# Kernel optimization log

Measured on AMD Instinct MI355X. Metric: run time of the kernel, lower is better.

Reference implementation:

```python
import jax, jax.numpy as jnp
import numpy as np

T_DIFF = 1000.0
LN_EPS = 1e-5


def _lin(x, w, b):
    return jnp.matmul(x, w.T) + b


def _ln(x, g, b):
    m = jnp.mean(x, axis=-1, keepdims=True)
    v = jnp.mean((x - m) ** 2, axis=-1, keepdims=True)
    return (x - m) / jnp.sqrt(v + LN_EPS) * g + b


def _pos_lin(x, w, b):
    return jnp.matmul(x, jax.nn.softplus(w).T) + b


def _gamma(t, g_l1_w, g_l1_b, g_l2_w, g_l2_b, g_l3_w, g_l3_b, gamma_0, gamma_1):
    def gtilde(u):
        l1 = _pos_lin(u, g_l1_w, g_l1_b)
        return l1 + _pos_lin(jax.nn.sigmoid(_pos_lin(l1, g_l2_w, g_l2_b)), g_l3_w, g_l3_b)
    g0, g1, gt = gtilde(jnp.zeros_like(t)), gtilde(jnp.ones_like(t)), gtilde(t)
    return gamma_0 + (gamma_1 - gamma_0) * (gt - g0) / (g1 - g0)


def _pair_dist(a):
    # safe pairwise euclidean distances, (B,N,N,1)
    diff = a[:, :, None, :] - a[:, None, :, :]
    d2 = jnp.sum(diff * diff, axis=-1, keepdims=True)
    return diff, jnp.sqrt(jnp.maximum(d2, 1e-12)), d2


def _egc_layer(x, h, x0, p):
    _, d0, _ = _pair_dist(x0)                      # original distances
    diff, dist, d2 = _pair_dist(x)                 # current distances (pre-LN x)
    h = _ln(h, p['lnh_g'], p['lnh_b'])
    x = _ln(x, p['lnx_g'], p['lnx_b'])
    B, N, F = h.shape
    h_i = jnp.broadcast_to(h[:, :, None, :], (B, N, N, F))
    h_j = jnp.broadcast_to(h[:, None, :, :], (B, N, N, F))
    einp = jnp.concatenate([h_i, h_j, d2, d0], axis=-1)  # (B,N,N,2F+2)
    m = jax.nn.silu(_lin(einp, p['edg1_w'], p['edg1_b']))
    m = jax.nn.silu(_lin(m, p['edg2_w'], p['edg2_b']))
    e = jax.nn.sigmoid(_lin(m, p['edgi_w'], p['edgi_b']))
    e = e * (1.0 - jnp.eye(N, dtype=e.dtype)[None, :, :, None])
    m_agg = jnp.sum(e * m, axis=2)                 # sum over j -> (B,N,F)
    hn = jax.nn.silu(_lin(jnp.concatenate([h, m_agg], axis=-1), p['node1_w'], p['node1_b']))
    hn = h + _lin(hn, p['node2_w'], p['node2_b'])
    cw = jax.nn.silu(_lin(einp, p['cor1_w'], p['cor1_b']))
    cw = jax.nn.silu(_lin(cw, p['cor2_w'], p['cor2_b']))
    cw = _lin(cw, p['cor3_w'], p['cor3_b'])        # (B,N,N,1)
    x_next = x + jnp.sum(cw * (diff / (dist + 1.0)), axis=2)
    return x_next, hn


def setup_inputs() -> dict:
    key = jax.random.key(0)
    ks = iter(jax.random.split(key, 64))
    B, N, H, L = 8, 192, 32, 4
    d = {}
    d['xyz_atom_species'] = jax.random.normal(next(ks), (B, N, 4), jnp.float32)
    d['pdf'] = jax.random.normal(next(ks), (B, 3000), jnp.float32)
    d['t'] = jax.random.uniform(next(ks), (B,), jnp.float32) * T_DIFF

    def w(k, shape):
        fan_in = shape[-1]
        return jax.random.normal(k, shape, jnp.float32) / np.sqrt(fan_in)

    d['emb_in_w'] = w(next(ks), (H, 12)); d['emb_in_b'] = jnp.zeros((H,), jnp.float32)
    d['emb_out_w'] = w(next(ks), (1, H)); d['emb_out_b'] = jnp.zeros((1,), jnp.float32)
    d['x_out_w'] = w(next(ks), (3, 3)); d['x_out_b'] = jnp.zeros((3,), jnp.float32)
    d['pdf_w'] = w(next(ks), (10, 3000)); d['pdf_b'] = jnp.zeros((10,), jnp.float32)
    d['g_l1_w'] = w(next(ks), (1, 1)); d['g_l1_b'] = jnp.zeros((1,), jnp.float32)
    d['g_l2_w'] = w(next(ks), (1024, 1)); d['g_l2_b'] = jnp.zeros((1024,), jnp.float32)
    d['g_l3_w'] = w(next(ks), (1, 1024)); d['g_l3_b'] = jnp.zeros((1,), jnp.float32)
    d['gamma_0'] = jnp.array([-5.0], jnp.float32)
    d['gamma_1'] = jnp.array([10.0], jnp.float32)
    d['lnh_g'] = jnp.ones((L, H), jnp.float32); d['lnh_b'] = jnp.zeros((L, H), jnp.float32)
    d['lnx_g'] = jnp.ones((L, 3), jnp.float32); d['lnx_b'] = jnp.zeros((L, 3), jnp.float32)
    d['edg1_w'] = w(next(ks), (L, H, 2 * H + 2)); d['edg1_b'] = jnp.zeros((L, H), jnp.float32)
    d['edg2_w'] = w(next(ks), (L, H, H)); d['edg2_b'] = jnp.zeros((L, H), jnp.float32)
    d['edgi_w'] = w(next(ks), (L, 1, H)); d['edgi_b'] = jnp.zeros((L, 1), jnp.float32)
    d['node1_w'] = w(next(ks), (L, H, 2 * H)); d['node1_b'] = jnp.zeros((L, H), jnp.float32)
    d['node2_w'] = w(next(ks), (L, H, H)); d['node2_b'] = jnp.zeros((L, H), jnp.float32)
    d['cor1_w'] = w(next(ks), (L, H, 2 * H + 2)); d['cor1_b'] = jnp.zeros((L, H), jnp.float32)
    d['cor2_w'] = w(next(ks), (L, H, H)); d['cor2_b'] = jnp.zeros((L, H), jnp.float32)
    d['cor3_w'] = w(next(ks), (L, 1, H)); d['cor3_b'] = jnp.zeros((L, 1), jnp.float32)
    return d


def reference(xyz_atom_species, pdf, t, emb_in_w, emb_in_b, emb_out_w, emb_out_b,
              x_out_w, x_out_b, pdf_w, pdf_b, g_l1_w, g_l1_b, g_l2_w, g_l2_b,
              g_l3_w, g_l3_b, gamma_0, gamma_1, lnh_g, lnh_b, lnx_g, lnx_b,
              edg1_w, edg1_b, edg2_w, edg2_b, edgi_w, edgi_b, node1_w, node1_b,
              node2_w, node2_b, cor1_w, cor1_b, cor2_w, cor2_b, cor3_w, cor3_b):
    B, N, _ = xyz_atom_species.shape
    h = xyz_atom_species[:, :, 3:4]                # (B,N,1)
    x = xyz_atom_species[:, :, :3]
    x0 = x
    tn = (t / T_DIFF)[:, None]                     # (B,1)
    t_emb = _gamma(tn, g_l1_w, g_l1_b, g_l2_w, g_l2_b, g_l3_w, g_l3_b, gamma_0, gamma_1)
    pdf_emb = _lin(pdf, pdf_w, pdf_b)              # (B,10)
    h = jnp.concatenate([
        h,
        jnp.broadcast_to(t_emb[:, None, :], (B, N, 1)),
        jnp.broadcast_to(pdf_emb[:, None, :], (B, N, 10)),
    ], axis=-1)
    h = _lin(h, emb_in_w, emb_in_b)                # (B,N,32)
    for l in range(4):
        p = dict(lnh_g=lnh_g[l], lnh_b=lnh_b[l], lnx_g=lnx_g[l], lnx_b=lnx_b[l],
                 edg1_w=edg1_w[l], edg1_b=edg1_b[l], edg2_w=edg2_w[l], edg2_b=edg2_b[l],
                 edgi_w=edgi_w[l], edgi_b=edgi_b[l], node1_w=node1_w[l], node1_b=node1_b[l],
                 node2_w=node2_w[l], node2_b=node2_b[l], cor1_w=cor1_w[l], cor1_b=cor1_b[l],
                 cor2_w=cor2_w[l], cor2_b=cor2_b[l], cor3_w=cor3_w[l], cor3_b=cor3_b[l])
        x, h = _egc_layer(x, h, x0, p)
    h = _lin(h, emb_out_w, emb_out_b)
    x = _lin(x, x_out_w, x_out_b) - x0
    return jnp.concatenate([x, h], axis=-1)        # (B,N,4)
```

## Files before the change

### kernel.cpp

```cpp
#include <hip/hip_runtime.h>
#include <hip/hip_bf16.h>
#include <math.h>

#define BATCH 8
#define NATOMS 192
#define HF 32

using short8 = __attribute__((ext_vector_type(8))) short;
using f32x4  = __attribute__((ext_vector_type(4))) float;

__device__ __forceinline__ float fast_rcp(float x){ return __builtin_amdgcn_rcpf(x); }
__device__ __forceinline__ float sigmoid_f(float x){ return fast_rcp(1.0f+__expf(-x)); }
__device__ __forceinline__ float silu_f(float x){ return x*fast_rcp(1.0f+__expf(-x)); }
__device__ __forceinline__ float softplus_f(float x){ return fmaxf(x,0.0f)+log1pf(expf(-fabsf(x))); }
__device__ __forceinline__ unsigned short f2bf(float x){
  __hip_bfloat16 h = __float2bfloat16(x);
  return __builtin_bit_cast(unsigned short, h);
}

__device__ __forceinline__ float wave_sum(float v){
  v += __shfl_xor(v, 1);
  v += __shfl_xor(v, 2);
  v += __shfl_xor(v, 4);
  v += __shfl_xor(v, 8);
  v += __shfl_xor(v, 16);
  v += __shfl_xor(v, 32);
  return v;
}

__global__ __launch_bounds__(256) void k_prelude(
    const float* __restrict__ pdf, const float* __restrict__ t,
    const float* __restrict__ pdf_w, const float* __restrict__ pdf_b,
    const float* __restrict__ g1w, const float* __restrict__ g1b,
    const float* __restrict__ g2w, const float* __restrict__ g2b,
    const float* __restrict__ g3w, const float* __restrict__ g3b,
    const float* __restrict__ gamma0, const float* __restrict__ gamma1,
    float* __restrict__ temb, float* __restrict__ pdfe)
{
  __shared__ float lds[4];
  const int bx = blockIdx.x, tid = threadIdx.x;
  const int wv = tid >> 6, ln = tid & 63;

  if (bx < 80){
    const int b = bx / 10, o = bx % 10;
    const float* pb = pdf + b*3000;
    const float* wb = pdf_w + o*3000;
    float p = 0.f;
    for (int k = tid; k < 3000; k += 256) p = fmaf(pb[k], wb[k], p);
    p = wave_sum(p);
    if (ln == 0) lds[wv] = p;
    __syncthreads();
    if (tid == 0) pdfe[b*10 + o] = lds[0] + lds[1] + lds[2] + lds[3] + pdf_b[o];
    return;
  }
  const int b = bx - 80;
  const float w1 = softplus_f(g1w[0]);
  const float b1 = g1b[0];
  const float tn = t[b] * (1.0f/1000.0f);
  const float l1_0 = b1;
  const float l1_1 = w1 + b1;
  const float l1_t = fmaf(w1, tn, b1);
  float a0 = 0.f, a1 = 0.f, at = 0.f;
  for (int k = tid; k < 1024; k += 256){
    float w2 = softplus_f(g2w[k]);
    float bb = g2b[k];
    float w3 = softplus_f(g3w[k]);
    a0 += sigmoid_f(fmaf(w2, l1_0, bb)) * w3;
    a1 += sigmoid_f(fmaf(w2, l1_1, bb)) * w3;
    at += sigmoid_f(fmaf(w2, l1_t, bb)) * w3;
  }
  float sums[3]; float vals[3] = {a0, a1, at};
  for (int r = 0; r < 3; ++r){
    float v = wave_sum(vals[r]);
    __syncthreads();
    if (ln == 0) lds[wv] = v;
    __syncthreads();
    sums[r] = lds[0] + lds[1] + lds[2] + lds[3];
  }
  if (tid == 0){
    const float b3 = g3b[0];
    const float g0 = l1_0 + sums[0] + b3;
    const float g1v = l1_1 + sums[1] + b3;
    const float gt = l1_t + sums[2] + b3;
    temb[b] = gamma0[0] + (gamma1[0] - gamma0[0]) * (gt - g0) / (g1v - g0);
  }
}

__global__ __launch_bounds__(256) void k_embed(
    const float* __restrict__ xyz, const float* __restrict__ temb,
    const float* __restrict__ pdfe, const float* __restrict__ wi,
    const float* __restrict__ bi, float* __restrict__ h, float* __restrict__ x)
{
  int g = blockIdx.x * 256 + threadIdx.x;
  if (g >= BATCH*NATOMS*HF) return;
  int f = g & 31;
  int node = g >> 5;
  int b = node / NATOMS;
  float sp = xyz[node*4 + 3];
  const float* w = wi + f*12;
  float a = bi[f];
  a = fmaf(sp, w[0], a);
  a = fmaf(temb[b], w[1], a);
  const float* pe = pdfe + b*10;
#pragma unroll
  for (int p = 0; p < 10; ++p) a = fmaf(pe[p], w[2+p], a);
  h[node*32 + f] = a;
  if (f < 3) x[node*3 + f] = xyz[node*4 + f];
}

__global__ __launch_bounds__(256) void k_wprep(
    const float* __restrict__ e2w, const float* __restrict__ c2w,
    unsigned short* __restrict__ e2wb, unsigned short* __restrict__ c2wb)
{
  int g = blockIdx.x*256 + threadIdx.x;
  if (g < 4096){
    e2wb[g] = f2bf(e2w[g]);
    c2wb[g] = f2bf(c2w[g]);
  }
}

__global__ __launch_bounds__(256) void k_node(
    const float* __restrict__ hraw,
    const float* __restrict__ lnhg, const float* __restrict__ lnhb,
    const float* __restrict__ e1w, const float* __restrict__ e1b,
    const float* __restrict__ c1w, const float* __restrict__ c1b,
    float* __restrict__ hln, float* __restrict__ ue, float* __restrict__ uc,
    float* __restrict__ vep, float* __restrict__ vcp)
{
  int g = blockIdx.x * 256 + threadIdx.x;
  if (g >= BATCH*NATOMS*32) return;
  const int f = g & 31, node = g >> 5;
  const float* row = hraw + node*32;
  float hl[32];
  float m = 0.f;
#pragma unroll
  for (int k = 0; k < 32; ++k){ hl[k] = row[k]; m += hl[k]; }
  m *= (1.0f/32.0f);
  float v = 0.f;
#pragma unroll
  for (int k = 0; k < 32; ++k){ float d = hl[k]-m; v = fmaf(d, d, v); }
  float r = rsqrtf(v*(1.0f/32.0f) + 1e-5f);
#pragma unroll
  for (int k = 0; k < 32; ++k) hl[k] = fmaf((hl[k]-m)*r, lnhg[k], lnhb[k]);
  hln[node*32 + f] = hl[f];

  const float* we = e1w + f*66;
  float sv = e1b[f], su = 0.f;
#pragma unroll
  for (int k = 0; k < 32; ++k){ sv = fmaf(hl[k], we[k], sv); su = fmaf(hl[k], we[32+k], su); }
  vep[node*32 + f] = sv;
  ue [node*32 + f] = su;

  const float* wc = c1w + f*66;
  float cv = c1b[f], cu = 0.f;
#pragma unroll
  for (int k = 0; k < 32; ++k){ cv = fmaf(hl[k], wc[k], cv); cu = fmaf(hl[k], wc[32+k], cu); }
  vcp[node*32 + f] = cv;
  uc [node*32 + f] = cu;
}

__global__ __launch_bounds__(128, 3) void k_pair(
    const float* __restrict__ xin, const float* __restrict__ xyz,
    const float* __restrict__ ue, const float* __restrict__ uc,
    const float* __restrict__ vep, const float* __restrict__ vcp,
    const float* __restrict__ e1w, const float* __restrict__ c1w,
    const unsigned short* __restrict__ e2wb, const unsigned short* __restrict__ c2wb,
    const float* __restrict__ e2b, const float* __restrict__ eiw,
    const float* __restrict__ eib,
    const float* __restrict__ c2b, const float* __restrict__ c3w,
    const float* __restrict__ c3b,
    float* __restrict__ pm, float* __restrict__ pxc)
{
  __shared__ float s_geo[64][6];
  __shared__ unsigned short s_m1[64][40];
  __shared__ unsigned short s_c1[64][40];
  __shared__ unsigned short s_we[32][40];
  __shared__ unsigned short s_wc[32][40];

  const int i = blockIdx.x, b = blockIdx.y, chunk = blockIdx.z;
  const int tid = threadIdx.x;
  const int base = b * NATOMS;

  if (tid < 64){
    const int jj = tid;
    const int j = chunk*64 + jj;
    const float* xi_p = xin + (base + i)*3;
    const float* xj_p = xin + (base + j)*3;
    const float dfx = xi_p[0] - xj_p[0], dfy = xi_p[1] - xj_p[1], dfz = xi_p[2] - xj_p[2];
    const float d2 = dfx*dfx + dfy*dfy + dfz*dfz;
    const float dist = sqrtf(fmaxf(d2, 1e-12f));
    const float* x0i = xyz + (base + i)*4;
    const float* x0j = xyz + (base + j)*4;
    const float q0 = x0i[0]-x0j[0], q1 = x0i[1]-x0j[1], q2 = x0i[2]-x0j[2];
    const float d0 = sqrtf(fmaxf(q0*q0 + q1*q1 + q2*q2, 1e-12f));
    s_geo[jj][0] = dfx; s_geo[jj][1] = dfy; s_geo[jj][2] = dfz;
    s_geo[jj][3] = d2;  s_geo[jj][4] = d0;  s_geo[jj][5] = dist;
  } else {
    const int u = tid - 64;
    const short8* es = (const short8*)e2wb;
    const short8* cs = (const short8*)c2wb;
#pragma unroll
    for (int h = 0; h < 2; ++h){
      const int c = u + h*64;
      const int f = c >> 2, kq = c & 3;
      *(short8*)&s_we[f][kq*8] = es[c];
      *(short8*)&s_wc[f][kq*8] = cs[c];
    }
  }
  __syncthreads();

  {
    const int k = tid & 31, jg = tid >> 5;
    const float vpe = vep[(base + i)*32 + k];
    const float vpc = vcp[(base + i)*32 + k];
    const float we64 = e1w[k*66 + 64], we65 = e1w[k*66 + 65];
    const float wc64 = c1w[k*66 + 64], wc65 = c1w[k*66 + 65];
#pragma unroll
    for (int jj = jg; jj < 64; jj += 4){
      const float d2 = s_geo[jj][3], d0 = s_geo[jj][4];
      const int j = chunk*64 + jj;
      const float uev = ue[(size_t)(base + j)*32 + k];
      const float m1 = silu_f(fmaf(d2, we64, fmaf(d0, we65, vpe + uev)));
      s_m1[jj][k] = f2bf(m1);
      const float ucv = uc[(size_t)(base + j)*32 + k];
      const float c1 = silu_f(fmaf(d2, wc64, fmaf(d0, wc65, vpc + ucv)));
      s_c1[jj][k] = f2bf(c1);
    }
  }
  __syncthreads();

  const int lane = tid & 63;
  const int n = lane & 15, quad = lane >> 4;

  if (tid < 64){
    short8 b0 = *(const short8*)&s_we[n][quad*8];
    short8 b1 = *(const short8*)&s_we[16 + n][quad*8];
    f32x4 acc0[4], acc1[4];
#pragma unroll
    for (int jt = 0; jt < 4; ++jt){
      short8 a = *(const short8*)&s_m1[jt*16 + n][quad*8];
      f32x4 z = {0.f, 0.f, 0.f, 0.f};
      acc0[jt] = __builtin_amdgcn_mfma_f32_16x16x32_bf16(a, b0, z, 0, 0, 0);
      acc1[jt] = __builtin_amdgcn_mfma_f32_16x16x32_bf16(a, b1, z, 0, 0, 0);
    }
    const float eb0 = e2b[n], eb1 = e2b[16 + n];
    const float ew0 = eiw[n], ew1 = eiw[16 + n];
    const float ebias = eib[0];
    float ma0 = 0.f, ma1 = 0.f;
#pragma unroll
    for (int jt = 0; jt < 4; ++jt){
      float m20[4], m21[4], g[4];
#pragma unroll
      for (int r = 0; r < 4; ++r){
        m20[r] = silu_f(acc0[jt][r] + eb0);
        m21[r] = silu_f(acc1[jt][r] + eb1);
        g[r] = m20[r]*ew0 + m21[r]*ew1;
      }
#pragma unroll
      for (int r = 0; r < 4; ++r){
        g[r] += __shfl_xor(g[r], 1);
        g[r] += __shfl_xor(g[r], 2);
        g[r] += __shfl_xor(g[r], 4);
        g[r] += __shfl_xor(g[r], 8);
      }
#pragma unroll
      for (int r = 0; r < 4; ++r){
        const int jglob = chunk*64 + jt*16 + quad*4 + r;
        const float e = (jglob == i) ? 0.0f : sigmoid_f(g[r] + ebias);
        ma0 = fmaf(e, m20[r], ma0);
        ma1 = fmaf(e, m21[r], ma1);
      }
    }
    ma0 += __shfl_xor(ma0, 16); ma0 += __shfl_xor(ma0, 32);
    ma1 += __shfl_xor(ma1, 16); ma1 += __shfl_xor(ma1, 32);
    if (lane < 16){
      float* o = pm + ((size_t)(base + i)*3 + chunk)*32;
      o[lane] = ma0;
      o[16 + lane] = ma1;
    }
  } else {
    short8 b0 = *(const short8*)&s_wc[n][quad*8];
    short8 b1 = *(const short8*)&s_wc[16 + n][quad*8];
    f32x4 acc0[4], acc1[4];
#pragma unroll
    for (int jt = 0; jt < 4; ++jt){
      short8 a = *(const short8*)&s_c1[jt*16 + n][quad*8];
      f32x4 z = {0.f, 0.f, 0.f, 0.f};
      acc0[jt] = __builtin_amdgcn_mfma_f32_16x16x32_bf16(a, b0, z, 0, 0, 0);
      acc1[jt] = __builtin_amdgcn_mfma_f32_16x16x32_bf16(a, b1, z, 0, 0, 0);
    }
    const float cb0 = c2b[n], cb1 = c2b[16 + n];
    const float cw0 = c3w[n], cw1 = c3w[16 + n];
    const float cbias = c3b[0];
    float px = 0.f, py = 0.f, pz = 0.f;
#pragma unroll
    for (int jt = 0; jt < 4; ++jt){
      float g[4];
#pragma unroll
      for (int r = 0; r < 4; ++r){
        g[r] = silu_f(acc0[jt][r] + cb0)*cw0 + silu_f(acc1[jt][r] + cb1)*cw1;
      }
#pragma unroll
      for (int r = 0; r < 4; ++r){
        g[r] += __shfl_xor(g[r], 1);
        g[r] += __shfl_xor(g[r], 2);
        g[r] += __shfl_xor(g[r], 4);
        g[r] += __shfl_xor(g[r], 8);
      }
#pragma unroll
      for (int r = 0; r < 4; ++r){
        const int jj = jt*16 + quad*4 + r;
        const float s = (g[r] + cbias) * fast_rcp(s_geo[jj][5] + 1.0f);
        px = fmaf(s, s_geo[jj][0], px);
        py = fmaf(s, s_geo[jj][1], py);
        pz = fmaf(s, s_geo[jj][2], pz);
      }
    }
    px += __shfl_xor(px, 16); px += __shfl_xor(px, 32);
    py += __shfl_xor(py, 16); py += __shfl_xor(py, 32);
    pz += __shfl_xor(pz, 16); pz += __shfl_xor(pz, 32);
    if (lane == 0){
      float* o = pxc + ((size_t)(base + i)*3 + chunk)*3;
      o[0] = px; o[1] = py; o[2] = pz;
    }
  }
}

__global__ __launch_bounds__(256) void k_post(
    float* hln, const float* __restrict__ xin,
    const float* __restrict__ pm, const float* __restrict__ pxc,
    float* __restrict__ hout, float* __restrict__ xout,
    const float* __restrict__ n1w, const float* __restrict__ n1b,
    const float* __restrict__ n2w, const float* __restrict__ n2b,
    const float* __restrict__ lnxg, const float* __restrict__ lnxb,
    const float* __restrict__ lnhg_n, const float* __restrict__ lnhb_n,
    const float* __restrict__ e1w_n, const float* __restrict__ e1b_n,
    const float* __restrict__ c1w_n, const float* __restrict__ c1b_n,
    float* __restrict__ ue, float* __restrict__ uc,
    float* __restrict__ vep, float* __restrict__ vcp)
{
  __shared__ float s_hl[8][33];
  __shared__ float s_mg[8][33];
  __shared__ float s_n1[8][33];
  __shared__ float s_ho[8][33];

  const int tid = threadIdx.x;
  const int il = tid >> 5, f = tid & 31;
  const int node = blockIdx.x*8 + il;

  const float hlf = hln[node*32 + f];
  s_hl[il][f] = hlf;
  const float* pmn = pm + (size_t)node*96;
  s_mg[il][f] = pmn[f] + pmn[32 + f] + pmn[64 + f];
  __syncthreads();

  float a = n1b[f];
  const float* w1 = n1w + f*64;
#pragma unroll
  for (int k = 0; k < 32; ++k) a = fmaf(s_hl[il][k], w1[k], a);
#pragma unroll
  for (int k = 0; k < 32; ++k) a = fmaf(s_mg[il][k], w1[32+k], a);
  s_n1[il][f] = silu_f(a);

  if (f < 3){
    const float* xr = xin + node*3;
    const float x0 = xr[0], x1 = xr[1], x2 = xr[2];
    const float mx = (x0 + x1 + x2) * (1.0f/3.0f);
    const float v0 = x0-mx, v1 = x1-mx, v2 = x2-mx;
    const float r = rsqrtf((v0*v0 + v1*v1 + v2*v2)*(1.0f/3.0f) + 1e-5f);
    const float xv = (f == 0) ? x0 : ((f == 1) ? x1 : x2);
    const float xl = fmaf((xv - mx)*r, lnxg[f], lnxb[f]);
    const float* pc = pxc + (size_t)node*9;
    xout[node*3 + f] = xl + pc[f] + pc[3 + f] + pc[6 + f];
  }
  __syncthreads();

  float o = n2b[f];
  const float* w2 = n2w + f*32;
#pragma unroll
  for (int k = 0; k < 32; ++k) o = fmaf(s_n1[il][k], w2[k], o);
  const float ho = hlf + o;
  hout[node*32 + f] = ho;
  s_ho[il][f] = ho;
  __syncthreads();

  float m = 0.f;
#pragma unroll
  for (int k = 0; k < 32; ++k) m += s_ho[il][k];
  m *= (1.0f/32.0f);
  float v = 0.f;
#pragma unroll
  for (int k = 0; k < 32; ++k){ float d = s_ho[il][k]-m; v = fmaf(d, d, v); }
  const float r = rsqrtf(v*(1.0f/32.0f) + 1e-5f);
  float hl[32];
#pragma unroll
  for (int k = 0; k < 32; ++k) hl[k] = fmaf((s_ho[il][k]-m)*r, lnhg_n[k], lnhb_n[k]);
  hln[node*32 + f] = hl[f];

  const float* we = e1w_n + f*66;
  float sv = e1b_n[f], su = 0.f;
#pragma unroll
  for (int k = 0; k < 32; ++k){ sv = fmaf(hl[k], we[k], sv); su = fmaf(hl[k], we[32+k], su); }
  vep[node*32 + f] = sv;
  ue [node*32 + f] = su;

  const float* wc = c1w_n + f*66;
  float cv = c1b_n[f], cu = 0.f;
#pragma unroll
  for (int k = 0; k < 32; ++k){ cv = fmaf(hl[k], wc[k], cv); cu = fmaf(hl[k], wc[32+k], cu); }
  vcp[node*32 + f] = cv;
  uc [node*32 + f] = cu;
}

__global__ __launch_bounds__(256) void k_final(
    const float* __restrict__ hin, const float* __restrict__ xin,
    const float* __restrict__ xyz,
    const float* __restrict__ how, const float* __restrict__ hob,
    const float* __restrict__ xow, const float* __restrict__ xob,
    float* __restrict__ out)
{
  int g = blockIdx.x * 256 + threadIdx.x;
  if (g >= BATCH*NATOMS) return;
  const float* h = hin + g*32;
  float a = hob[0];
#pragma unroll
  for (int k = 0; k < 32; ++k) a = fmaf(h[k], how[k], a);
  const float* x = xin + g*3;
#pragma unroll
  for (int c = 0; c < 3; ++c){
    float o = xob[c];
    o = fmaf(x[0], xow[c*3+0], o);
    o = fmaf(x[1], xow[c*3+1], o);
    o = fmaf(x[2], xow[c*3+2], o);
    out[g*4 + c] = o - xyz[g*4 + c];
  }
  out[g*4 + 3] = a;
}

extern "C" void kernel_launch(void* const* d_in, const int* in_sizes, int n_in,
                              void* d_out, int out_size, void* d_ws, size_t ws_size,
                              hipStream_t stream)
{
  const float* xyz      = (const float*)d_in[0];
  const float* pdf      = (const float*)d_in[1];
  const float* t        = (const float*)d_in[2];
  const float* emb_in_w = (const float*)d_in[3];
  const float* emb_in_b = (const float*)d_in[4];
  const float* emb_out_w= (const float*)d_in[5];
  const float* emb_out_b= (const float*)d_in[6];
  const float* x_out_w  = (const float*)d_in[7];
  const float* x_out_b  = (const float*)d_in[8];
  const float* pdf_w    = (const float*)d_in[9];
  const float* pdf_b    = (const float*)d_in[10];
  const float* g1w      = (const float*)d_in[11];
  const float* g1b      = (const float*)d_in[12];
  const float* g2w      = (const float*)d_in[13];
  const float* g2b      = (const float*)d_in[14];
  const float* g3w      = (const float*)d_in[15];
  const float* g3b      = (const float*)d_in[16];
  const float* gamma0   = (const float*)d_in[17];
  const float* gamma1   = (const float*)d_in[18];
  const float* lnhg     = (const float*)d_in[19];
  const float* lnhb     = (const float*)d_in[20];
  const float* lnxg     = (const float*)d_in[21];
  const float* lnxb     = (const float*)d_in[22];
  const float* e1w      = (const float*)d_in[23];
  const float* e1b      = (const float*)d_in[24];
  const float* e2w      = (const float*)d_in[25];
  const float* e2b      = (const float*)d_in[26];
  const float* eiw      = (const float*)d_in[27];
  const float* eib      = (const float*)d_in[28];
  const float* n1w      = (const float*)d_in[29];
  const float* n1b      = (const float*)d_in[30];
  const float* n2w      = (const float*)d_in[31];
  const float* n2b      = (const float*)d_in[32];
  const float* c1w      = (const float*)d_in[33];
  const float* c1b      = (const float*)d_in[34];
  const float* c2w      = (const float*)d_in[35];
  const float* c2b      = (const float*)d_in[36];
  const float* c3w      = (const float*)d_in[37];
  const float* c3b      = (const float*)d_in[38];

  const int NTOT = BATCH*NATOMS;
  float* ws   = (float*)d_ws;
  float* temb = ws;
  float* pdfe = ws + 8;
  unsigned short* e2wb = (unsigned short*)(ws + 96);
  unsigned short* c2wb = e2wb + 4096;
  float* h0   = ws + 96 + 4096;
  float* hout = h0   + NTOT*32;
  float* xb0  = hout + NTOT*32;
  float* xb1  = xb0  + NTOT*3;
  float* hln  = xb1  + NTOT*3;
  float* ue   = hln  + NTOT*32;
  float* uc   = ue   + NTOT*32;
  float* vep  = uc   + NTOT*32;
  float* vcp  = vep  + NTOT*32;
  float* pm   = vcp  + NTOT*32;
  float* pxc  = pm   + NTOT*96;

  k_prelude<<<88, 256, 0, stream>>>(pdf, t, pdf_w, pdf_b,
      g1w, g1b, g2w, g2b, g3w, g3b, gamma0, gamma1, temb, pdfe);
  k_embed<<<(NTOT*HF + 255)/256, 256, 0, stream>>>(
      xyz, temb, pdfe, emb_in_w, emb_in_b, h0, xb0);
  k_wprep<<<16, 256, 0, stream>>>(e2w, c2w, e2wb, c2wb);
  k_node<<<(NTOT*32 + 255)/256, 256, 0, stream>>>(
      h0, lnhg, lnhb, e1w, e1b, c1w, c1b, hln, ue, uc, vep, vcp);

  const float* xcur = xb0; float* xnext = xb1;
  for (int l = 0; l < 4; ++l){
    const int n = (l < 3) ? (l + 1) : 3;
    k_pair<<<dim3(NATOMS, BATCH, 3), 128, 0, stream>>>(
        xcur, xyz, ue, uc, vep, vcp,
        e1w + l*2112, c1w + l*2112,
        e2wb + l*1024, c2wb + l*1024,
        e2b + l*32, eiw + l*32, eib + l,
        c2b + l*32, c3w + l*32, c3b + l,
        pm, pxc);
    k_post<<<NTOT/8, 256, 0, stream>>>(
        hln, xcur, pm, pxc, hout, xnext,
        n1w + l*2048, n1b + l*32, n2w + l*1024, n2b + l*32,
        lnxg + l*3, lnxb + l*3,
        lnhg + n*32, lnhb + n*32, e1w + n*2112, e1b + n*32,
        c1w + n*2112, c1b + n*32,
        ue, uc, vep, vcp);
    const float* tx = xcur; xcur = xnext; xnext = (float*)tx;
  }

  k_final<<<(NTOT + 255)/256, 256, 0, stream>>>(
      hout, xcur, xyz, emb_out_w, emb_out_b, x_out_w, x_out_b, (float*)d_out);
}
```

Measured before the change: 274.0 us.

## Fuse pair and post kernels per layer, merge prelude/embed/node launches

```diff
diff --git a/kernel.cpp b/kernel.cpp
--- a/kernel.cpp
+++ b/kernel.cpp
@@ -35,12 +35,20 @@
     const float* __restrict__ g2w, const float* __restrict__ g2b,
     const float* __restrict__ g3w, const float* __restrict__ g3b,
     const float* __restrict__ gamma0, const float* __restrict__ gamma1,
-    float* __restrict__ temb, float* __restrict__ pdfe)
+    const float* __restrict__ e2w, const float* __restrict__ c2w,
+    float* __restrict__ temb, float* __restrict__ pdfe,
+    unsigned short* __restrict__ e2wb, unsigned short* __restrict__ c2wb)
 {
   __shared__ float lds[4];
   const int bx = blockIdx.x, tid = threadIdx.x;
   const int wv = tid >> 6, ln = tid & 63;
 
+  if (bx >= 88){
+    const int g = (bx - 88)*256 + tid;
+    e2wb[g] = f2bf(e2w[g]);
+    c2wb[g] = f2bf(c2w[g]);
+    return;
+  }
   if (bx < 80){
     const int b = bx / 10, o = bx % 10;
     const float* pb = pdf + b*3000;
@@ -86,55 +94,37 @@
   }
 }
 
-__global__ __launch_bounds__(256) void k_embed(
+__global__ __launch_bounds__(256) void k_embed_node(
     const float* __restrict__ xyz, const float* __restrict__ temb,
-    const float* __restrict__ pdfe, const float* __restrict__ wi,
-    const float* __restrict__ bi, float* __restrict__ h, float* __restrict__ x)
-{
-  int g = blockIdx.x * 256 + threadIdx.x;
-  if (g >= BATCH*NATOMS*HF) return;
-  int f = g & 31;
-  int node = g >> 5;
-  int b = node / NATOMS;
-  float sp = xyz[node*4 + 3];
-  const float* w = wi + f*12;
-  float a = bi[f];
-  a = fmaf(sp, w[0], a);
-  a = fmaf(temb[b], w[1], a);
-  const float* pe = pdfe + b*10;
-#pragma unroll
-  for (int p = 0; p < 10; ++p) a = fmaf(pe[p], w[2+p], a);
-  h[node*32 + f] = a;
-  if (f < 3) x[node*3 + f] = xyz[node*4 + f];
-}
-
-__global__ __launch_bounds__(256) void k_wprep(
-    const float* __restrict__ e2w, const float* __restrict__ c2w,
-    unsigned short* __restrict__ e2wb, unsigned short* __restrict__ c2wb)
-{
-  int g = blockIdx.x*256 + threadIdx.x;
-  if (g < 4096){
-    e2wb[g] = f2bf(e2w[g]);
-    c2wb[g] = f2bf(c2w[g]);
-  }
-}
-
-__global__ __launch_bounds__(256) void k_node(
-    const float* __restrict__ hraw,
+    const float* __restrict__ pdfe,
+    const float* __restrict__ wi, const float* __restrict__ bi,
     const float* __restrict__ lnhg, const float* __restrict__ lnhb,
     const float* __restrict__ e1w, const float* __restrict__ e1b,
     const float* __restrict__ c1w, const float* __restrict__ c1b,
-    float* __restrict__ hln, float* __restrict__ ue, float* __restrict__ uc,
+    float* __restrict__ x, float* __restrict__ hln,
+    float* __restrict__ ue, float* __restrict__ uc,
     float* __restrict__ vep, float* __restrict__ vcp)
 {
-  int g = blockIdx.x * 256 + threadIdx.x;
-  if (g >= BATCH*NATOMS*32) return;
-  const int f = g & 31, node = g >> 5;
-  const float* row = hraw + node*32;
+  __shared__ float s_h[8][33];
+  const int tid = threadIdx.x;
+  const int il = tid >> 5, f = tid & 31;
+  const int node = blockIdx.x*8 + il;
+  const int b = node / NATOMS;
+  const float* w = wi + f*12;
+  float a = bi[f];
+  a = fmaf(xyz[node*4 + 3], w[0], a);
+  a = fmaf(temb[b], w[1], a);
+  const float* pe = pdfe + b*10;
+#pragma unroll
+  for (int p = 0; p < 10; ++p) a = fmaf(pe[p], w[2+p], a);
+  s_h[il][f] = a;
+  if (f < 3) x[node*3 + f] = xyz[node*4 + f];
+  __syncthreads();
+
   float hl[32];
   float m = 0.f;
 #pragma unroll
-  for (int k = 0; k < 32; ++k){ hl[k] = row[k]; m += hl[k]; }
+  for (int k = 0; k < 32; ++k){ hl[k] = s_h[il][k]; m += hl[k]; }
   m *= (1.0f/32.0f);
   float v = 0.f;
 #pragma unroll
@@ -159,282 +149,260 @@
   uc [node*32 + f] = cu;
 }
 
-__global__ __launch_bounds__(128, 3) void k_pair(
+__global__ __launch_bounds__(128, 3) void k_layer(
     const float* __restrict__ xin, const float* __restrict__ xyz,
     const float* __restrict__ ue, const float* __restrict__ uc,
     const float* __restrict__ vep, const float* __restrict__ vcp,
+    const float* __restrict__ hln,
     const float* __restrict__ e1w, const float* __restrict__ c1w,
     const unsigned short* __restrict__ e2wb, const unsigned short* __restrict__ c2wb,
     const float* __restrict__ e2b, const float* __restrict__ eiw,
     const float* __restrict__ eib,
     const float* __restrict__ c2b, const float* __restrict__ c3w,
     const float* __restrict__ c3b,
-    float* __restrict__ pm, float* __restrict__ pxc)
-{
-  __shared__ float s_geo[64][6];
-  __shared__ unsigned short s_m1[64][40];
-  __shared__ unsigned short s_c1[64][40];
-  __shared__ unsigned short s_we[32][40];
-  __shared__ unsigned short s_wc[32][40];
-
-  const int i = blockIdx.x, b = blockIdx.y, chunk = blockIdx.z;
-  const int tid = threadIdx.x;
-  const int base = b * NATOMS;
-
-  if (tid < 64){
-    const int jj = tid;
-    const int j = chunk*64 + jj;
-    const float* xi_p = xin + (base + i)*3;
-    const float* xj_p = xin + (base + j)*3;
-    const float dfx = xi_p[0] - xj_p[0], dfy = xi_p[1] - xj_p[1], dfz = xi_p[2] - xj_p[2];
-    const float d2 = dfx*dfx + dfy*dfy + dfz*dfz;
-    const float dist = sqrtf(fmaxf(d2, 1e-12f));
-    const float* x0i = xyz + (base + i)*4;
-    const float* x0j = xyz + (base + j)*4;
-    const float q0 = x0i[0]-x0j[0], q1 = x0i[1]-x0j[1], q2 = x0i[2]-x0j[2];
-    const float d0 = sqrtf(fmaxf(q0*q0 + q1*q1 + q2*q2, 1e-12f));
-    s_geo[jj][0] = dfx; s_geo[jj][1] = dfy; s_geo[jj][2] = dfz;
-    s_geo[jj][3] = d2;  s_geo[jj][4] = d0;  s_geo[jj][5] = dist;
-  } else {
-    const int u = tid - 64;
-    const short8* es = (const short8*)e2wb;
-    const short8* cs = (const short8*)c2wb;
-#pragma unroll
-    for (int h = 0; h < 2; ++h){
-      const int c = u + h*64;
-      const int f = c >> 2, kq = c & 3;
-      *(short8*)&s_we[f][kq*8] = es[c];
-      *(short8*)&s_wc[f][kq*8] = cs[c];
-    }
-  }
-  __syncthreads();
-
-  {
-    const int k = tid & 31, jg = tid >> 5;
-    const float vpe = vep[(base + i)*32 + k];
-    const float vpc = vcp[(base + i)*32 + k];
-    const float we64 = e1w[k*66 + 64], we65 = e1w[k*66 + 65];
-    const float wc64 = c1w[k*66 + 64], wc65 = c1w[k*66 + 65];
-#pragma unroll
-    for (int jj = jg; jj < 64; jj += 4){
-      const float d2 = s_geo[jj][3], d0 = s_geo[jj][4];
-      const int j = chunk*64 + jj;
-      const float uev = ue[(size_t)(base + j)*32 + k];
-      const float m1 = silu_f(fmaf(d2, we64, fmaf(d0, we65, vpe + uev)));
-      s_m1[jj][k] = f2bf(m1);
-      const float ucv = uc[(size_t)(base + j)*32 + k];
-      const float c1 = silu_f(fmaf(d2, wc64, fmaf(d0, wc65, vpc + ucv)));
-      s_c1[jj][k] = f2bf(c1);
-    }
-  }
-  __syncthreads();
-
-  const int lane = tid & 63;
-  const int n = lane & 15, quad = lane >> 4;
-
-  if (tid < 64){
-    short8 b0 = *(const short8*)&s_we[n][quad*8];
-    short8 b1 = *(const short8*)&s_we[16 + n][quad*8];
-    f32x4 acc0[4], acc1[4];
-#pragma unroll
-    for (int jt = 0; jt < 4; ++jt){
-      short8 a = *(const short8*)&s_m1[jt*16 + n][quad*8];
-      f32x4 z = {0.f, 0.f, 0.f, 0.f};
-      acc0[jt] = __builtin_amdgcn_mfma_f32_16x16x32_bf16(a, b0, z, 0, 0, 0);
-      acc1[jt] = __builtin_amdgcn_mfma_f32_16x16x32_bf16(a, b1, z, 0, 0, 0);
-    }
-    const float eb0 = e2b[n], eb1 = e2b[16 + n];
-    const float ew0 = eiw[n], ew1 = eiw[16 + n];
-    const float ebias = eib[0];
-    float ma0 = 0.f, ma1 = 0.f;
-#pragma unroll
-    for (int jt = 0; jt < 4; ++jt){
-      float m20[4], m21[4], g[4];
-#pragma unroll
-      for (int r = 0; r < 4; ++r){
-        m20[r] = silu_f(acc0[jt][r] + eb0);
-        m21[r] = silu_f(acc1[jt][r] + eb1);
-        g[r] = m20[r]*ew0 + m21[r]*ew1;
-      }
-#pragma unroll
-      for (int r = 0; r < 4; ++r){
-        g[r] += __shfl_xor(g[r], 1);
-        g[r] += __shfl_xor(g[r], 2);
-        g[r] += __shfl_xor(g[r], 4);
-        g[r] += __shfl_xor(g[r], 8);
-      }
-#pragma unroll
-      for (int r = 0; r < 4; ++r){
-        const int jglob = chunk*64 + jt*16 + quad*4 + r;
-        const float e = (jglob == i) ? 0.0f : sigmoid_f(g[r] + ebias);
-        ma0 = fmaf(e, m20[r], ma0);
-        ma1 = fmaf(e, m21[r], ma1);
-      }
-    }
-    ma0 += __shfl_xor(ma0, 16); ma0 += __shfl_xor(ma0, 32);
-    ma1 += __shfl_xor(ma1, 16); ma1 += __shfl_xor(ma1, 32);
-    if (lane < 16){
-      float* o = pm + ((size_t)(base + i)*3 + chunk)*32;
-      o[lane] = ma0;
-      o[16 + lane] = ma1;
-    }
-  } else {
-    short8 b0 = *(const short8*)&s_wc[n][quad*8];
-    short8 b1 = *(const short8*)&s_wc[16 + n][quad*8];
-    f32x4 acc0[4], acc1[4];
-#pragma unroll
-    for (int jt = 0; jt < 4; ++jt){
-      short8 a = *(const short8*)&s_c1[jt*16 + n][quad*8];
-      f32x4 z = {0.f, 0.f, 0.f, 0.f};
-      acc0[jt] = __builtin_amdgcn_mfma_f32_16x16x32_bf16(a, b0, z, 0, 0, 0);
-      acc1[jt] = __builtin_amdgcn_mfma_f32_16x16x32_bf16(a, b1, z, 0, 0, 0);
-    }
-    const float cb0 = c2b[n], cb1 = c2b[16 + n];
-    const float cw0 = c3w[n], cw1 = c3w[16 + n];
-    const float cbias = c3b[0];
-    float px = 0.f, py = 0.f, pz = 0.f;
-#pragma unroll
-    for (int jt = 0; jt < 4; ++jt){
-      float g[4];
-#pragma unroll
-      for (int r = 0; r < 4; ++r){
-        g[r] = silu_f(acc0[jt][r] + cb0)*cw0 + silu_f(acc1[jt][r] + cb1)*cw1;
-      }
-#pragma unroll
-      for (int r = 0; r < 4; ++r){
-        g[r] += __shfl_xor(g[r], 1);
-        g[r] += __shfl_xor(g[r], 2);
-        g[r] += __shfl_xor(g[r], 4);
-        g[r] += __shfl_xor(g[r], 8);
-      }
-#pragma unroll
-      for (int r = 0; r < 4; ++r){
-        const int jj = jt*16 + quad*4 + r;
-        const float s = (g[r] + cbias) * fast_rcp(s_geo[jj][5] + 1.0f);
-        px = fmaf(s, s_geo[jj][0], px);
-        py = fmaf(s, s_geo[jj][1], py);
-        pz = fmaf(s, s_geo[jj][2], pz);
-      }
-    }
-    px += __shfl_xor(px, 16); px += __shfl_xor(px, 32);
-    py += __shfl_xor(py, 16); py += __shfl_xor(py, 32);
-    pz += __shfl_xor(pz, 16); pz += __shfl_xor(pz, 32);
-    if (lane == 0){
-      float* o = pxc + ((size_t)(base + i)*3 + chunk)*3;
-      o[0] = px; o[1] = py; o[2] = pz;
-    }
-  }
-}
-
-__global__ __launch_bounds__(256) void k_post(
-    float* hln, const float* __restrict__ xin,
-    const float* __restrict__ pm, const float* __restrict__ pxc,
-    float* __restrict__ hout, float* __restrict__ xout,
     const float* __restrict__ n1w, const float* __restrict__ n1b,
     const float* __restrict__ n2w, const float* __restrict__ n2b,
     const float* __restrict__ lnxg, const float* __restrict__ lnxb,
     const float* __restrict__ lnhg_n, const float* __restrict__ lnhb_n,
     const float* __restrict__ e1w_n, const float* __restrict__ e1b_n,
     const float* __restrict__ c1w_n, const float* __restrict__ c1b_n,
-    float* __restrict__ ue, float* __restrict__ uc,
-    float* __restrict__ vep, float* __restrict__ vcp)
+    float* __restrict__ xout, float* __restrict__ hln_n,
+    float* __restrict__ ue_n, float* __restrict__ uc_n,
+    float* __restrict__ vep_n, float* __restrict__ vcp_n,
+    const float* __restrict__ how, const float* __restrict__ hob,
+    const float* __restrict__ xow, const float* __restrict__ xob,
+    float* __restrict__ out, int last)
 {
-  __shared__ float s_hl[8][33];
-  __shared__ float s_mg[8][33];
-  __shared__ float s_n1[8][33];
-  __shared__ float s_ho[8][33];
-
+  __shared__ float s_geo[192][6];
+  __shared__ unsigned short s_m1[64][40];
+  __shared__ unsigned short s_c1[64][40];
+  __shared__ unsigned short s_we[32][40];
+  __shared__ unsigned short s_wc[32][40];
+  __shared__ float s_mg[32];
+  __shared__ float s_hv[32];
+  __shared__ float s_n1[32];
+  __shared__ float s_hl[32];
+
+  const int i = blockIdx.x, b = blockIdx.y;
   const int tid = threadIdx.x;
-  const int il = tid >> 5, f = tid & 31;
-  const int node = blockIdx.x*8 + il;
-
-  const float hlf = hln[node*32 + f];
-  s_hl[il][f] = hlf;
-  const float* pmn = pm + (size_t)node*96;
-  s_mg[il][f] = pmn[f] + pmn[32 + f] + pmn[64 + f];
+  const int base = b * NATOMS;
+
+  {
+    const float* xi_p = xin + (size_t)(base + i)*3;
+    const float xi0 = xi_p[0], xi1 = xi_p[1], xi2 = xi_p[2];
+    const float* x0i = xyz + (size_t)(base + i)*4;
+    const float q0i = x0i[0], q1i = x0i[1], q2i = x0i[2];
+    for (int j = tid; j < NATOMS; j += 128){
+      const float* xj_p = xin + (size_t)(base + j)*3;
+      const float dfx = xi0 - xj_p[0], dfy = xi1 - xj_p[1], dfz = xi2 - xj_p[2];
+      const float d2 = dfx*dfx + dfy*dfy + dfz*dfz;
+      const float dist = sqrtf(fmaxf(d2, 1e-12f));
+      const float* x0j = xyz + (size_t)(base + j)*4;
+      const float q0 = q0i - x0j[0], q1 = q1i - x0j[1], q2 = q2i - x0j[2];
+      const float d0 = sqrtf(fmaxf(q0*q0 + q1*q1 + q2*q2, 1e-12f));
+      s_geo[j][0] = dfx; s_geo[j][1] = dfy; s_geo[j][2] = dfz;
+      s_geo[j][3] = d2;  s_geo[j][4] = d0;  s_geo[j][5] = dist;
+    }
+    const short8* es = (const short8*)e2wb;
+    const short8* cs = (const short8*)c2wb;
+    const int f = tid >> 2, kq = tid & 3;
+    *(short8*)&s_we[f][kq*8] = es[tid];
+    *(short8*)&s_wc[f][kq*8] = cs[tid];
+  }
   __syncthreads();
 
-  float a = n1b[f];
-  const float* w1 = n1w + f*64;
-#pragma unroll
-  for (int k = 0; k < 32; ++k) a = fmaf(s_hl[il][k], w1[k], a);
-#pragma unroll
-  for (int k = 0; k < 32; ++k) a = fmaf(s_mg[il][k], w1[32+k], a);
-  s_n1[il][f] = silu_f(a);
-
-  if (f < 3){
-    const float* xr = xin + node*3;
+  const int kk = tid & 31, jg = tid >> 5;
+  const float vpe = vep[(size_t)(base + i)*32 + kk];
+  const float vpc = vcp[(size_t)(base + i)*32 + kk];
+  const float we64 = e1w[kk*66 + 64], we65 = e1w[kk*66 + 65];
+  const float wc64 = c1w[kk*66 + 64], wc65 = c1w[kk*66 + 65];
+
+  const int lane = tid & 63, wv = tid >> 6;
+  const int n = lane & 15, quad = lane >> 4;
+  short8 wb0, wb1;
+  float p0s, p1s, p2s, p3s, p4s;
+  if (wv == 0){
+    wb0 = *(const short8*)&s_we[n][quad*8];
+    wb1 = *(const short8*)&s_we[16 + n][quad*8];
+    p0s = e2b[n]; p1s = e2b[16 + n]; p2s = eiw[n]; p3s = eiw[16 + n]; p4s = eib[0];
+  } else {
+    wb0 = *(const short8*)&s_wc[n][quad*8];
+    wb1 = *(const short8*)&s_wc[16 + n][quad*8];
+    p0s = c2b[n]; p1s = c2b[16 + n]; p2s = c3w[n]; p3s = c3w[16 + n]; p4s = c3b[0];
+  }
+  float ma0 = 0.f, ma1 = 0.f;
+  float px = 0.f, py = 0.f, pz = 0.f;
+
+  for (int c = 0; c < 3; ++c){
+#pragma unroll
+    for (int jj = jg; jj < 64; jj += 4){
+      const int j = c*64 + jj;
+      const float d2 = s_geo[j][3], d0 = s_geo[j][4];
+      const float uev = ue[(size_t)(base + j)*32 + kk];
+      s_m1[jj][kk] = f2bf(silu_f(fmaf(d2, we64, fmaf(d0, we65, vpe + uev))));
+      const float ucv = uc[(size_t)(base + j)*32 + kk];
+      s_c1[jj][kk] = f2bf(silu_f(fmaf(d2, wc64, fmaf(d0, wc65, vpc + ucv))));
+    }
+    __syncthreads();
+
+    if (wv == 0){
+#pragma unroll
+      for (int jt = 0; jt < 4; ++jt){
+        short8 a = *(const short8*)&s_m1[jt*16 + n][quad*8];
+        f32x4 z = {0.f, 0.f, 0.f, 0.f};
+        f32x4 A0 = __builtin_amdgcn_mfma_f32_16x16x32_bf16(a, wb0, z, 0, 0, 0);
+        f32x4 A1 = __builtin_amdgcn_mfma_f32_16x16x32_bf16(a, wb1, z, 0, 0, 0);
+        float m20[4], m21[4], g[4];
+#pragma unroll
+        for (int r = 0; r < 4; ++r){
+          m20[r] = silu_f(A0[r] + p0s);
+          m21[r] = silu_f(A1[r] + p1s);
+          g[r] = m20[r]*p2s + m21[r]*p3s;
+        }
+#pragma unroll
+        for (int r = 0; r < 4; ++r){
+          g[r] += __shfl_xor(g[r], 1);
+          g[r] += __shfl_xor(g[r], 2);
+          g[r] += __shfl_xor(g[r], 4);
+          g[r] += __shfl_xor(g[r], 8);
+        }
+#pragma unroll
+        for (int r = 0; r < 4; ++r){
+          const int jglob = c*64 + jt*16 + quad*4 + r;
+          const float e = (jglob == i) ? 0.0f : sigmoid_f(g[r] + p4s);
+          ma0 = fmaf(e, m20[r], ma0);
+          ma1 = fmaf(e, m21[r], ma1);
+        }
+      }
+    } else {
+#pragma unroll
+      for (int jt = 0; jt < 4; ++jt){
+        short8 a = *(const short8*)&s_c1[jt*16 + n][quad*8];
+        f32x4 z = {0.f, 0.f, 0.f, 0.f};
+        f32x4 A0 = __builtin_amdgcn_mfma_f32_16x16x32_bf16(a, wb0, z, 0, 0, 0);
+        f32x4 A1 = __builtin_amdgcn_mfma_f32_16x16x32_bf16(a, wb1, z, 0, 0, 0);
+        float g[4];
+#pragma unroll
+        for (int r = 0; r < 4; ++r)
+          g[r] = silu_f(A0[r] + p0s)*p2s + silu_f(A1[r] + p1s)*p3s;
+#pragma unroll
+        for (int r = 0; r < 4; ++r){
+          g[r] += __shfl_xor(g[r], 1);
+          g[r] += __shfl_xor(g[r], 2);
+          g[r] += __shfl_xor(g[r], 4);
+          g[r] += __shfl_xor(g[r], 8);
+        }
+#pragma unroll
+        for (int r = 0; r < 4; ++r){
+          const int jgeo = c*64 + jt*16 + quad*4 + r;
+          const float s = (g[r] + p4s) * fast_rcp(s_geo[jgeo][5] + 1.0f);
+          px = fmaf(s, s_geo[jgeo][0], px);
+          py = fmaf(s, s_geo[jgeo][1], py);
+          pz = fmaf(s, s_geo[jgeo][2], pz);
+        }
+      }
+    }
+    __syncthreads();
+  }
+
+  if (wv == 0){
+    ma0 += __shfl_xor(ma0, 16); ma0 += __shfl_xor(ma0, 32);
+    ma1 += __shfl_xor(ma1, 16); ma1 += __shfl_xor(ma1, 32);
+    if (lane < 16){ s_mg[lane] = ma0; s_mg[16 + lane] = ma1; }
+  } else {
+    px += __shfl_xor(px, 16); px += __shfl_xor(px, 32);
+    py += __shfl_xor(py, 16); py += __shfl_xor(py, 32);
+    pz += __shfl_xor(pz, 16); pz += __shfl_xor(pz, 32);
+    if (lane < 32) s_hv[lane] = hln[(size_t)(base + i)*32 + lane];
+  }
+  __syncthreads();
+
+  if (wv == 0){
+    if (lane < 32){
+      const int f = lane;
+      float a = n1b[f];
+      const float* w1 = n1w + f*64;
+#pragma unroll
+      for (int k = 0; k < 32; ++k) a = fmaf(s_hv[k], w1[k], a);
+#pragma unroll
+      for (int k = 0; k < 32; ++k) a = fmaf(s_mg[k], w1[32+k], a);
+      s_n1[f] = silu_f(a);
+    }
+  } else {
+    const float* xr = xin + (size_t)(base + i)*3;
     const float x0 = xr[0], x1 = xr[1], x2 = xr[2];
     const float mx = (x0 + x1 + x2) * (1.0f/3.0f);
     const float v0 = x0-mx, v1 = x1-mx, v2 = x2-mx;
     const float r = rsqrtf((v0*v0 + v1*v1 + v2*v2)*(1.0f/3.0f) + 1e-5f);
-    const float xv = (f == 0) ? x0 : ((f == 1) ? x1 : x2);
-    const float xl = fmaf((xv - mx)*r, lnxg[f], lnxb[f]);
-    const float* pc = pxc + (size_t)node*9;
-    xout[node*3 + f] = xl + pc[f] + pc[3 + f] + pc[6 + f];
+    const float xn0 = fmaf((x0 - mx)*r, lnxg[0], lnxb[0]) + px;
+    const float xn1 = fmaf((x1 - mx)*r, lnxg[1], lnxb[1]) + py;
+    const float xn2 = fmaf((x2 - mx)*r, lnxg[2], lnxb[2]) + pz;
+    if (!last){
+      if (lane == 0){
+        float* xo = xout + (size_t)(base + i)*3;
+        xo[0] = xn0; xo[1] = xn1; xo[2] = xn2;
+      }
+    } else if (lane < 3){
+      float o = xob[lane];
+      o = fmaf(xn0, xow[lane*3 + 0], o);
+      o = fmaf(xn1, xow[lane*3 + 1], o);
+      o = fmaf(xn2, xow[lane*3 + 2], o);
+      out[(size_t)(base + i)*4 + lane] = o - xyz[(size_t)(base + i)*4 + lane];
+    }
   }
   __syncthreads();
 
-  float o = n2b[f];
-  const float* w2 = n2w + f*32;
-#pragma unroll
-  for (int k = 0; k < 32; ++k) o = fmaf(s_n1[il][k], w2[k], o);
-  const float ho = hlf + o;
-  hout[node*32 + f] = ho;
-  s_ho[il][f] = ho;
-  __syncthreads();
-
-  float m = 0.f;
-#pragma unroll
-  for (int k = 0; k < 32; ++k) m += s_ho[il][k];
-  m *= (1.0f/32.0f);
-  float v = 0.f;
-#pragma unroll
-  for (int k = 0; k < 32; ++k){ float d = s_ho[il][k]-m; v = fmaf(d, d, v); }
-  const float r = rsqrtf(v*(1.0f/32.0f) + 1e-5f);
-  float hl[32];
-#pragma unroll
-  for (int k = 0; k < 32; ++k) hl[k] = fmaf((s_ho[il][k]-m)*r, lnhg_n[k], lnhb_n[k]);
-  hln[node*32 + f] = hl[f];
-
-  const float* we = e1w_n + f*66;
-  float sv = e1b_n[f], su = 0.f;
-#pragma unroll
-  for (int k = 0; k < 32; ++k){ sv = fmaf(hl[k], we[k], sv); su = fmaf(hl[k], we[32+k], su); }
-  vep[node*32 + f] = sv;
-  ue [node*32 + f] = su;
-
-  const float* wc = c1w_n + f*66;
-  float cv = c1b_n[f], cu = 0.f;
-#pragma unroll
-  for (int k = 0; k < 32; ++k){ cv = fmaf(hl[k], wc[k], cv); cu = fmaf(hl[k], wc[32+k], cu); }
-  vcp[node*32 + f] = cv;
-  uc [node*32 + f] = cu;
-}
-
-__global__ __launch_bounds__(256) void k_final(
-    const float* __restrict__ hin, const float* __restrict__ xin,
-    const float* __restrict__ xyz,
-    const float* __restrict__ how, const float* __restrict__ hob,
-    const float* __restrict__ xow, const float* __restrict__ xob,
-    float* __restrict__ out)
-{
-  int g = blockIdx.x * 256 + threadIdx.x;
-  if (g >= BATCH*NATOMS) return;
-  const float* h = hin + g*32;
-  float a = hob[0];
-#pragma unroll
-  for (int k = 0; k < 32; ++k) a = fmaf(h[k], how[k], a);
-  const float* x = xin + g*3;
-#pragma unroll
-  for (int c = 0; c < 3; ++c){
-    float o = xob[c];
-    o = fmaf(x[0], xow[c*3+0], o);
-    o = fmaf(x[1], xow[c*3+1], o);
-    o = fmaf(x[2], xow[c*3+2], o);
-    out[g*4 + c] = o - xyz[g*4 + c];
-  }
-  out[g*4 + 3] = a;
+  if (wv == 0 && lane < 32){
+    const int f = lane;
+    float o = n2b[f];
+    const float* w2 = n2w + f*32;
+#pragma unroll
+    for (int k = 0; k < 32; ++k) o = fmaf(s_n1[k], w2[k], o);
+    const float ho = s_hv[f] + o;
+    if (last){
+      float hp = ho * how[f];
+      hp += __shfl_xor(hp, 1); hp += __shfl_xor(hp, 2);
+      hp += __shfl_xor(hp, 4); hp += __shfl_xor(hp, 8);
+      hp += __shfl_xor(hp, 16);
+      if (f == 0) out[(size_t)(base + i)*4 + 3] = hp + hob[0];
+    } else {
+      float m = ho;
+      m += __shfl_xor(m, 1); m += __shfl_xor(m, 2);
+      m += __shfl_xor(m, 4); m += __shfl_xor(m, 8);
+      m += __shfl_xor(m, 16);
+      m *= (1.0f/32.0f);
+      const float d = ho - m;
+      float v = d*d;
+      v += __shfl_xor(v, 1); v += __shfl_xor(v, 2);
+      v += __shfl_xor(v, 4); v += __shfl_xor(v, 8);
+      v += __shfl_xor(v, 16);
+      const float r = rsqrtf(v*(1.0f/32.0f) + 1e-5f);
+      const float hlv = fmaf(d*r, lnhg_n[f], lnhb_n[f]);
+      s_hl[f] = hlv;
+      hln_n[(size_t)(base + i)*32 + f] = hlv;
+    }
+  }
+  if (!last){
+    __syncthreads();
+    if (lane < 32){
+      const int f = lane;
+      if (wv == 0){
+        const float* we = e1w_n + f*66;
+        float sv = e1b_n[f], su = 0.f;
+#pragma unroll
+        for (int k = 0; k < 32; ++k){ sv = fmaf(s_hl[k], we[k], sv); su = fmaf(s_hl[k], we[32+k], su); }
+        vep_n[(size_t)(base + i)*32 + f] = sv;
+        ue_n [(size_t)(base + i)*32 + f] = su;
+      } else {
+        const float* wc = c1w_n + f*66;
+        float cv = c1b_n[f], cu = 0.f;
+#pragma unroll
+        for (int k = 0; k < 32; ++k){ cv = fmaf(s_hl[k], wc[k], cv); cu = fmaf(s_hl[k], wc[32+k], cu); }
+        vcp_n[(size_t)(base + i)*32 + f] = cv;
+        uc_n [(size_t)(base + i)*32 + f] = cu;
+      }
+    }
+  }
 }
 
 extern "C" void kernel_launch(void* const* d_in, const int* in_sizes, int n_in,
@@ -487,46 +455,55 @@
   float* pdfe = ws + 8;
   unsigned short* e2wb = (unsigned short*)(ws + 96);
   unsigned short* c2wb = e2wb + 4096;
-  float* h0   = ws + 96 + 4096;
-  float* hout = h0   + NTOT*32;
-  float* xb0  = hout + NTOT*32;
-  float* xb1  = xb0  + NTOT*3;
-  float* hln  = xb1  + NTOT*3;
-  float* ue   = hln  + NTOT*32;
-  float* uc   = ue   + NTOT*32;
-  float* vep  = uc   + NTOT*32;
-  float* vcp  = vep  + NTOT*32;
-  float* pm   = vcp  + NTOT*32;
-  float* pxc  = pm   + NTOT*96;
-
-  k_prelude<<<88, 256, 0, stream>>>(pdf, t, pdf_w, pdf_b,
-      g1w, g1b, g2w, g2b, g3w, g3b, gamma0, gamma1, temb, pdfe);
-  k_embed<<<(NTOT*HF + 255)/256, 256, 0, stream>>>(
-      xyz, temb, pdfe, emb_in_w, emb_in_b, h0, xb0);
-  k_wprep<<<16, 256, 0, stream>>>(e2w, c2w, e2wb, c2wb);
-  k_node<<<(NTOT*32 + 255)/256, 256, 0, stream>>>(
-      h0, lnhg, lnhb, e1w, e1b, c1w, c1b, hln, ue, uc, vep, vcp);
-
-  const float* xcur = xb0; float* xnext = xb1;
+  float* p    = ws + 96 + 4096;
+  float* hln0 = p; p += NTOT*32;
+  float* hln1 = p; p += NTOT*32;
+  float* ue0  = p; p += NTOT*32;
+  float* uc0  = p; p += NTOT*32;
+  float* vep0 = p; p += NTOT*32;
+  float* vcp0 = p; p += NTOT*32;
+  float* ue1  = p; p += NTOT*32;
+  float* uc1  = p; p += NTOT*32;
+  float* vep1 = p; p += NTOT*32;
+  float* vcp1 = p; p += NTOT*32;
+  float* xb0  = p; p += NTOT*3;
+  float* xb1  = p; p += NTOT*3;
+
+  k_prelude<<<104, 256, 0, stream>>>(pdf, t, pdf_w, pdf_b,
+      g1w, g1b, g2w, g2b, g3w, g3b, gamma0, gamma1,
+      e2w, c2w, temb, pdfe, e2wb, c2wb);
+  k_embed_node<<<NTOT/8, 256, 0, stream>>>(
+      xyz, temb, pdfe, emb_in_w, emb_in_b,
+      lnhg, lnhb, e1w, e1b, c1w, c1b,
+      xb0, hln0, ue0, uc0, vep0, vcp0);
+
+  float* hlnC = hln0; float* hlnN = hln1;
+  float* ueC = ue0, *ucC = uc0, *vepC = vep0, *vcpC = vcp0;
+  float* ueN = ue1, *ucN = uc1, *vepN = vep1, *vcpN = vcp1;
+  float* xcur = xb0; float* xnext = xb1;
+
   for (int l = 0; l < 4; ++l){
     const int n = (l < 3) ? (l + 1) : 3;
-    k_pair<<<dim3(NATOMS, BATCH, 3), 128, 0, stream>>>(
-        xcur, xyz, ue, uc, vep, vcp,
+    k_layer<<<dim3(NATOMS, BATCH), 128, 0, stream>>>(
+        xcur, xyz, ueC, ucC, vepC, vcpC, hlnC,
         e1w + l*2112, c1w + l*2112,
         e2wb + l*1024, c2wb + l*1024,
         e2b + l*32, eiw + l*32, eib + l,
         c2b + l*32, c3w + l*32, c3b + l,
-        pm, pxc);
-    k_post<<<NTOT/8, 256, 0, stream>>>(
-        hln, xcur, pm, pxc, hout, xnext,
         n1w + l*2048, n1b + l*32, n2w + l*1024, n2b + l*32,
         lnxg + l*3, lnxb + l*3,
         lnhg + n*32, lnhb + n*32, e1w + n*2112, e1b + n*32,
         c1w + n*2112, c1b + n*32,
-        ue, uc, vep, vcp);
-    const float* tx = xcur; xcur = xnext; xnext = (float*)tx;
-  }
-
-  k_final<<<(NTOT + 255)/256, 256, 0, stream>>>(
-      hout, xcur, xyz, emb_out_w, emb_out_b, x_out_w, x_out_b, (float*)d_out);
+        xnext, hlnN, ueN, ucN, vepN, vcpN,
+        emb_out_w, emb_out_b, x_out_w, x_out_b, (float*)d_out,
+        (l == 3) ? 1 : 0);
+    { float* tp;
+      tp = hlnC; hlnC = hlnN; hlnN = tp;
+      tp = ueC;  ueC  = ueN;  ueN  = tp;
+      tp = ucC;  ucC  = ucN;  ucN  = tp;
+      tp = vepC; vepC = vepN; vepN = tp;
+      tp = vcpC; vcpC = vcpN; vcpN = tp;
+      tp = xcur; xcur = xnext; xnext = tp;
+    }
+  }
 }
```

After: 270.7 us. Within noise of the previous version (-1.2%).
